# Optimization experiments

Measured on AMD Instinct MI355X. Metric: run time of the kernel, lower is better.

Reference implementation:

```python
import math
import jax, jax.numpy as jnp
import numpy as np

NUM_HEADS = 12
NUM_LANDMARKS = 32

def iterative_inv(mat, n_iter=6):
    # mat: [B, H, m, m] row-stochastic kernel; Newton-Schulz pseudo-inverse
    m = mat.shape[-1]
    I = jnp.eye(m, dtype=mat.dtype)
    K = mat
    # 'else' branch: per-(B,H) normalization by max column sum
    denom = jnp.max(jnp.sum(K, axis=-2), axis=-1)[..., None, None]
    V = jnp.swapaxes(K, -1, -2) / denom
    for _ in range(n_iter):
        KV = jnp.matmul(K, V)
        V = jnp.matmul(0.25 * V, 13.0 * I - jnp.matmul(KV, 15.0 * I - jnp.matmul(KV, 7.0 * I - KV)))
    return V

def setup_inputs() -> dict:
    key = jax.random.key(0)
    k1, k2, k3 = jax.random.split(key, 3)
    B, N, C = 8, 2048, 768
    x = jax.random.normal(k1, (B, N, C), dtype=jnp.float32)
    w_qkv = jax.random.normal(k2, (C, 3 * C), dtype=jnp.float32) * (1.0 / math.sqrt(C))
    w_proj = jax.random.normal(k3, (C, C), dtype=jnp.float32) * (1.0 / math.sqrt(C))
    b_proj = jnp.zeros((C,), dtype=jnp.float32)
    return {"x": x, "w_qkv": w_qkv, "w_proj": w_proj, "b_proj": b_proj}

def reference(x, w_qkv, w_proj, b_proj):
    B, N, C = x.shape
    H = NUM_HEADS
    d = C // H
    m = NUM_LANDMARKS
    qkv = (x @ w_qkv).reshape(B, N, 3, H, d).transpose(2, 0, 3, 1, 4)  # [3,B,H,N,d]
    Q, K, V = qkv[0], qkv[1], qkv[2]
    scale = 1.0 / math.sqrt(math.sqrt(d))
    Q = Q * scale
    K = K * scale
    # landmark pooling: mean over contiguous chunks of size N//m
    Q_l = Q.reshape(B, H, m, N // m, d).mean(axis=-2)  # [B,H,m,d]
    K_l = K.reshape(B, H, m, N // m, d).mean(axis=-2)
    kernel_1 = jax.nn.softmax(jnp.einsum('bhnd,bhmd->bhnm', Q, K_l), axis=-1)   # [B,H,N,m]
    kernel_2 = jax.nn.softmax(jnp.einsum('bhmd,bhkd->bhmk', Q_l, K_l), axis=-1) # [B,H,m,m]
    kernel_3 = jax.nn.softmax(jnp.einsum('bhmd,bhnd->bhmn', Q_l, K), axis=-1)   # [B,H,m,N]
    X = jnp.matmul(jnp.matmul(kernel_1, iterative_inv(kernel_2)), jnp.matmul(kernel_3, V))  # [B,H,N,d]
    X = X.transpose(0, 2, 1, 3).reshape(B, N, C)
    return X @ w_proj + b_proj
```

## Files before the change

### kernel.cpp

```cpp
#include <hip/hip_runtime.h>
#include <hip/hip_bf16.h>

typedef __hip_bfloat16 bf16;
typedef __attribute__((ext_vector_type(8))) __bf16 bf16x8;
typedef __attribute__((ext_vector_type(4))) float f32x4;

#define NB 8
#define SEQ 2048
#define CH 768
#define NH 12
#define HD 64
#define NL 32
#define BHT (NB*NH)
#define TOK (NB*SEQ)
#define QK_SCALE 0.35355339059327379f

#define BAR() __builtin_amdgcn_s_barrier()
#define WLGKM0() __asm__ __volatile__("s_waitcnt lgkmcnt(0)" ::: "memory")
#define WVM(n) __asm__ __volatile__("s_waitcnt vmcnt(" #n ")" ::: "memory")

__device__ __forceinline__ void async_ld16(const bf16* g, bf16* l) {
    unsigned loff = (unsigned)__builtin_amdgcn_readfirstlane((int)(unsigned)(uintptr_t)l);
    __builtin_amdgcn_global_load_lds(
        (const __attribute__((address_space(1))) unsigned*)(uintptr_t)g,
        (__attribute__((address_space(3))) unsigned*)(uintptr_t)loff, 16, 0, 0);
}

__global__ void convert_x(const float* __restrict__ x, bf16* __restrict__ xb) {
    size_t i = ((size_t)blockIdx.x * 256 + threadIdx.x) * 8;
    float4 a = *reinterpret_cast<const float4*>(x + i);
    float4 b = *reinterpret_cast<const float4*>(x + i + 4);
    alignas(16) bf16 tmp[8];
    tmp[0] = __float2bfloat16(a.x); tmp[1] = __float2bfloat16(a.y);
    tmp[2] = __float2bfloat16(a.z); tmp[3] = __float2bfloat16(a.w);
    tmp[4] = __float2bfloat16(b.x); tmp[5] = __float2bfloat16(b.y);
    tmp[6] = __float2bfloat16(b.z); tmp[7] = __float2bfloat16(b.w);
    *reinterpret_cast<uint4*>(xb + i) = *reinterpret_cast<const uint4*>(tmp);
}

__global__ void transpose_f32(const float* __restrict__ in, bf16* __restrict__ outp,
                              int Hrows, int Wcols) {
    __shared__ float tile[32][33];
    int bx = blockIdx.x * 32, by = blockIdx.y * 32;
    int tx = threadIdx.x, ty = threadIdx.y;
    for (int i = 0; i < 32; i += 8)
        tile[ty + i][tx] = in[(size_t)(by + ty + i) * Wcols + bx + tx];
    __syncthreads();
    for (int i = 0; i < 32; i += 8)
        outp[(size_t)(bx + ty + i) * Hrows + by + tx] = __float2bfloat16(tile[tx][ty + i]);
}

template <int EPI>
__global__ __launch_bounds__(512, 2) void gemm_bt(
    const bf16* __restrict__ A, const bf16* __restrict__ Bt,
    int Nout, int Kdim,
    bf16* __restrict__ q, bf16* __restrict__ k, bf16* __restrict__ vt,
    float* __restrict__ Ql, float* __restrict__ Kl,
    float* __restrict__ outp, const float* __restrict__ bias_f) {
    __shared__ __align__(16) bf16 As[2][256 * 64];
    __shared__ __align__(16) bf16 Bs[2][256 * 64];
    const int t = threadIdx.x;
    const int wave = t >> 6, lane = t & 63;
    const int quad = lane >> 4, l15 = lane & 15;
    const int wr = wave >> 2, wc = wave & 3;

    int p = blockIdx.y * gridDim.x + blockIdx.x;
    int xcd = p & 7, j = p >> 3;
    int gx = gridDim.x;
    int bn = j % gx;
    int bm = (j / gx) * 8 + xcd;
    const int bm0 = bm * 256;
    const int bn0 = bn * 256;

    const int T = Kdim >> 6;

    const int srow = t >> 3;
    const int scol = (((t & 7) ^ (srow & 7)) << 3);
    const bf16* Abase = A + (size_t)(bm0 + srow) * Kdim + scol;
    const bf16* Bbase = Bt + (size_t)(bn0 + srow) * Kdim + scol;

    auto stageA = [&](int kt, int hf) {
        const bf16* g = Abase + (size_t)(hf * 128) * Kdim + kt * 64;
        bf16* l = &As[kt & 1][hf * 8192 + t * 8];
        async_ld16(g, l);
        async_ld16(g + (size_t)64 * Kdim, l + 4096);
    };
    auto stageB = [&](int kt, int hf) {
        const bf16* g = Bbase + (size_t)(hf * 128) * Kdim + kt * 64;
        bf16* l = &Bs[kt & 1][hf * 8192 + t * 8];
        async_ld16(g, l);
        async_ld16(g + (size_t)64 * Kdim, l + 4096);
    };

    const int swk[2] = { (quad ^ (l15 & 7)) << 3, ((4 + quad) ^ (l15 & 7)) << 3 };
    const bf16* arow = &As[0][wr * 8192 + l15 * 64];
    const bf16* brow = &Bs[0][(wc >> 1) * 8192 + ((wc & 1) * 64 + l15) * 64];

    f32x4 acc[8][4];
    const f32x4 zero4 = {0.f, 0.f, 0.f, 0.f};
    #pragma unroll
    for (int i = 0; i < 8; i++)
        #pragma unroll
        for (int jj = 0; jj < 4; jj++) acc[i][jj] = zero4;

    stageA(0, 0); stageA(0, 1); stageB(0, 0); stageB(0, 1);
    if (T > 1) {
        stageB(1, 0); stageB(1, 1);
        WVM(4);
    } else {
        WVM(0);
    }
    BAR();

    bf16x8 a[4][2], b[4][2];
    #pragma unroll 2
    for (int kt = 0; kt < T; kt++) {
        const int cur = kt & 1;
        const bf16* ab = arow + cur * 16384;
        const bf16* bb = brow + cur * 16384;

        #pragma unroll
        for (int mi = 0; mi < 4; mi++)
            #pragma unroll
            for (int kk = 0; kk < 2; kk++)
                a[mi][kk] = *reinterpret_cast<const bf16x8*>(ab + mi * 1024 + swk[kk]);
        #pragma unroll
        for (int ni = 0; ni < 2; ni++)
            #pragma unroll
            for (int kk = 0; kk < 2; kk++)
                b[ni][kk] = *reinterpret_cast<const bf16x8*>(bb + ni * 1024 + swk[kk]);
        if (kt + 1 < T) stageA(kt + 1, 0);
        BAR(); WLGKM0();
        __builtin_amdgcn_s_setprio(1);
        #pragma unroll
        for (int mi = 0; mi < 4; mi++)
            #pragma unroll
            for (int ni = 0; ni < 2; ni++)
                #pragma unroll
                for (int kk = 0; kk < 2; kk++)
                    acc[mi][ni] = __builtin_amdgcn_mfma_f32_16x16x32_bf16(a[mi][kk], b[ni][kk], acc[mi][ni], 0, 0, 0);
        __builtin_amdgcn_s_setprio(0);
        BAR();

        #pragma unroll
        for (int ni = 2; ni < 4; ni++)
            #pragma unroll
            for (int kk = 0; kk < 2; kk++)
                b[ni][kk] = *reinterpret_cast<const bf16x8*>(bb + ni * 1024 + swk[kk]);
        if (kt + 1 < T) stageA(kt + 1, 1);
        BAR(); WLGKM0();
        __builtin_amdgcn_s_setprio(1);
        #pragma unroll
        for (int mi = 0; mi < 4; mi++)
            #pragma unroll
            for (int ni = 2; ni < 4; ni++)
                #pragma unroll
                for (int kk = 0; kk < 2; kk++)
                    acc[mi][ni] = __builtin_amdgcn_mfma_f32_16x16x32_bf16(a[mi][kk], b[ni][kk], acc[mi][ni], 0, 0, 0);
        __builtin_amdgcn_s_setprio(0);
        BAR();

        #pragma unroll
        for (int mi = 0; mi < 4; mi++)
            #pragma unroll
            for (int kk = 0; kk < 2; kk++)
                a[mi][kk] = *reinterpret_cast<const bf16x8*>(ab + (mi + 4) * 1024 + swk[kk]);
        if (kt + 2 < T) stageB(kt + 2, 0);
        BAR(); WLGKM0();
        __builtin_amdgcn_s_setprio(1);
        #pragma unroll
        for (int mi = 0; mi < 4; mi++)
            #pragma unroll
            for (int ni = 0; ni < 2; ni++)
                #pragma unroll
                for (int kk = 0; kk < 2; kk++)
                    acc[mi + 4][ni] = __builtin_amdgcn_mfma_f32_16x16x32_bf16(a[mi][kk], b[ni][kk], acc[mi + 4][ni], 0, 0, 0);
        __builtin_amdgcn_s_setprio(0);
        BAR();

        if (kt + 2 < T) stageB(kt + 2, 1);
        BAR(); WLGKM0();
        __builtin_amdgcn_s_setprio(1);
        #pragma unroll
        for (int mi = 0; mi < 4; mi++)
            #pragma unroll
            for (int ni = 2; ni < 4; ni++)
                #pragma unroll
                for (int kk = 0; kk < 2; kk++)
                    acc[mi + 4][ni] = __builtin_amdgcn_mfma_f32_16x16x32_bf16(a[mi][kk], b[ni][kk], acc[mi + 4][ni], 0, 0, 0);
        __builtin_amdgcn_s_setprio(0);
        if (kt + 2 < T) {
            WVM(4);
        } else if (kt + 1 < T) {
            WVM(0);
        }
        BAR();
    }

    if (EPI == 0) {
        const int which = bn0 / CH;
        const int rem0 = bn0 - which * CH + wc * 64;
        const int b = bm0 >> 11;
        const int h = rem0 >> 6;
        const int bh = b * NH + h;
        const int nnb = (bm0 & 2047) + wr * 128;
        if (which < 2) {
            bf16* dstqk = (which == 0) ? q : k;
            float* dstl = (which == 0) ? Ql : Kl;
            const int la0 = nnb >> 6;
            #pragma unroll
            for (int hf = 0; hf < 2; hf++) {
                #pragma unroll
                for (int ni = 0; ni < 4; ni++) {
                    int dd = ni * 16 + l15;
                    float colsum = 0.f;
                    #pragma unroll
                    for (int m2 = 0; m2 < 4; m2++) {
                        int mi = hf * 4 + m2;
                        int nn0 = nnb + mi * 16 + quad * 4;
                        #pragma unroll
                        for (int r = 0; r < 4; r++) {
                            float val = acc[mi][ni][r];
                            colsum += val;
                            dstqk[((size_t)bh * SEQ + nn0 + r) * HD + dd] = __float2bfloat16(val * QK_SCALE);
                        }
                    }
                    colsum += __shfl_xor(colsum, 16);
                    colsum += __shfl_xor(colsum, 32);
                    if (quad == 0)
                        dstl[((size_t)bh * NL + la0 + hf) * HD + dd] = colsum * (QK_SCALE / 64.f);
                }
            }
        } else {
            #pragma unroll
            for (int ni = 0; ni < 4; ni++) {
                int dd = ni * 16 + l15;
                #pragma unroll
                for (int mi = 0; mi < 8; mi++) {
                    int nn0 = nnb + mi * 16 + quad * 4;
                    alignas(8) bf16 four[4];
                    #pragma unroll
                    for (int r = 0; r < 4; r++) four[r] = __float2bfloat16(acc[mi][ni][r]);
                    *reinterpret_cast<uint2*>(&vt[((size_t)bh * HD + dd) * SEQ + nn0]) =
                        *reinterpret_cast<const uint2*>(four);
                }
            }
        }
    } else {
        #pragma unroll
        for (int ni = 0; ni < 4; ni++) {
            int col = bn0 + wc * 64 + ni * 16 + l15;
            float bb = bias_f[col];
            #pragma unroll
            for (int mi = 0; mi < 8; mi++)
                #pragma unroll
                for (int r = 0; r < 4; r++) {
                    int row = bm0 + wr * 128 + mi * 16 + quad * 4 + r;
                    outp[(size_t)row * Nout + col] = acc[mi][ni][r] + bb;
                }
        }
    }
}

__global__ __launch_bounds__(256) void k3_pv(const float* __restrict__ Ql,
                                             const bf16* __restrict__ Kb,
                                             const bf16* __restrict__ Vt,
                                             float* __restrict__ Opart,
                                             float* __restrict__ Spart) {
    __shared__ __align__(16) bf16 Pw[4][32 * 136];
    __shared__ __align__(16) float Ored[4][32 * 65];
    __shared__ float Sred[4 * 32];
    const int bh = blockIdx.x, cc = blockIdx.y;
    const int n0 = cc * 512;
    const int t = threadIdx.x;
    const int w = t >> 6, lane = t & 63;
    const int quad = lane >> 4, l15 = lane & 15;

    const bf16* Kbh = Kb + (size_t)bh * SEQ * HD;
    const bf16* Vtb = Vt + (size_t)bh * HD * SEQ;

    bf16x8 af[2][2];
    #pragma unroll
    for (int mt = 0; mt < 2; mt++)
        #pragma unroll
        for (int kh = 0; kh < 2; kh++) {
            const float* src = Ql + (size_t)bh * NL * HD + (mt * 16 + l15) * 64 + kh * 32 + quad * 8;
            alignas(16) bf16 tmp[8];
            #pragma unroll
            for (int jj = 0; jj < 8; jj++) tmp[jj] = __float2bfloat16(src[jj]);
            af[mt][kh] = *reinterpret_cast<const bf16x8*>(tmp);
        }

    const f32x4 zero4 = {0.f, 0.f, 0.f, 0.f};
    f32x4 oacc[2][4];
    #pragma unroll
    for (int mt = 0; mt < 2; mt++)
        #pragma unroll
        for (int nd = 0; nd < 4; nd++) oacc[mt][nd] = zero4;
    float rs[2][4];
    #pragma unroll
    for (int mt = 0; mt < 2; mt++)
        #pragma unroll
        for (int r = 0; r < 4; r++) rs[mt][r] = 0.f;

    bf16* Pme = &Pw[w][0];

    #pragma unroll
    for (int h = 0; h < 2; h++) {
        f32x4 sacc[2][4];
        #pragma unroll
        for (int mt = 0; mt < 2; mt++)
            #pragma unroll
            for (int nt = 0; nt < 4; nt++) sacc[mt][nt] = zero4;
        #pragma unroll
        for (int nt = 0; nt < 4; nt++) {
            int n = n0 + w * 128 + h * 64 + nt * 16 + l15;
            bf16x8 kf0 = *reinterpret_cast<const bf16x8*>(&Kbh[(size_t)n * HD + quad * 8]);
            bf16x8 kf1 = *reinterpret_cast<const bf16x8*>(&Kbh[(size_t)n * HD + 32 + quad * 8]);
            #pragma unroll
            for (int mt = 0; mt < 2; mt++) {
                sacc[mt][nt] = __builtin_amdgcn_mfma_f32_16x16x32_bf16(af[mt][0], kf0, sacc[mt][nt], 0, 0, 0);
                sacc[mt][nt] = __builtin_amdgcn_mfma_f32_16x16x32_bf16(af[mt][1], kf1, sacc[mt][nt], 0, 0, 0);
            }
        }
        #pragma unroll
        for (int mt = 0; mt < 2; mt++)
            #pragma unroll
            for (int nt = 0; nt < 4; nt++)
                #pragma unroll
                for (int r = 0; r < 4; r++) {
                    float pv = __expf(sacc[mt][nt][r]);
                    rs[mt][r] += pv;
                    int row = mt * 16 + quad * 4 + r;
                    Pme[row * 136 + h * 64 + nt * 16 + l15] = __float2bfloat16(pv);
                }
    }
    __asm__ __volatile__("s_waitcnt lgkmcnt(0)" ::: "memory");

    #pragma unroll
    for (int kt = 0; kt < 4; kt++) {
        bf16x8 pa[2];
        pa[0] = *reinterpret_cast<const bf16x8*>(&Pme[l15 * 136 + kt * 32 + quad * 8]);
        pa[1] = *reinterpret_cast<const bf16x8*>(&Pme[(16 + l15) * 136 + kt * 32 + quad * 8]);
        int kbase = n0 + w * 128 + kt * 32 + quad * 8;
        #pragma unroll
        for (int nd = 0; nd < 4; nd++) {
            bf16x8 bv = *reinterpret_cast<const bf16x8*>(&Vtb[(size_t)(nd * 16 + l15) * SEQ + kbase]);
            oacc[0][nd] = __builtin_amdgcn_mfma_f32_16x16x32_bf16(pa[0], bv, oacc[0][nd], 0, 0, 0);
            oacc[1][nd] = __builtin_amdgcn_mfma_f32_16x16x32_bf16(pa[1], bv, oacc[1][nd], 0, 0, 0);
        }
    }

    #pragma unroll
    for (int mt = 0; mt < 2; mt++)
        #pragma unroll
        for (int r = 0; r < 4; r++) {
            float v = rs[mt][r];
            #pragma unroll
            for (int o = 1; o < 16; o <<= 1) v += __shfl_xor(v, o);
            rs[mt][r] = v;
        }
    if (l15 == 0)
        #pragma unroll
        for (int mt = 0; mt < 2; mt++)
            #pragma unroll
            for (int r = 0; r < 4; r++)
                Sred[w * 32 + mt * 16 + quad * 4 + r] = rs[mt][r];
    #pragma unroll
    for (int mt = 0; mt < 2; mt++)
        #pragma unroll
        for (int nd = 0; nd < 4; nd++)
            #pragma unroll
            for (int r = 0; r < 4; r++)
                Ored[w][(mt * 16 + quad * 4 + r) * 65 + nd * 16 + l15] = oacc[mt][nd][r];
    __syncthreads();

    float* Op = Opart + ((size_t)bh * 4 + cc) * (NL * HD);
    for (int e = t; e < 2048; e += 256) {
        int m = e >> 6, dd = e & 63;
        Op[e] = Ored[0][m * 65 + dd] + Ored[1][m * 65 + dd] +
                Ored[2][m * 65 + dd] + Ored[3][m * 65 + dd];
    }
    if (t < 32)
        Spart[((size_t)bh * 4 + cc) * NL + t] = Sred[t] + Sred[32 + t] + Sred[64 + t] + Sred[96 + t];
}

__device__ inline void mm32(float* Cm, const float* Am, const float* Bm, int t) {
    for (int e = t; e < 1024; e += 256) {
        int i = e >> 5, jj = e & 31;
        float s = 0.f;
        #pragma unroll
        for (int kk = 0; kk < 32; kk++) s += Am[i * 32 + kk] * Bm[kk * 32 + jj];
        Cm[e] = s;
    }
}

__global__ __launch_bounds__(256) void newton_inv(const float* __restrict__ Ql,
                                                  const float* __restrict__ Kl,
                                                  const float* __restrict__ Opart,
                                                  const float* __restrict__ Spart,
                                                  float* __restrict__ W2) {
    __shared__ float K2[1024], Vv[1024], KV[1024], Ta[1024], Tb[1024];
    __shared__ float K3[2048];
    __shared__ float stot[32];
    __shared__ float red[32];
    __shared__ float denom_s;
    int bh = blockIdx.x;
    int t = threadIdx.x;
    const float* ql = Ql + (size_t)bh * NL * HD;
    const float* kl = Kl + (size_t)bh * NL * HD;

    if (t < 32) {
        const float* sp = Spart + (size_t)bh * 4 * NL;
        stot[t] = sp[t] + sp[32 + t] + sp[64 + t] + sp[96 + t];
    }
    {
        const float* op = Opart + (size_t)bh * 4 * (NL * HD);
        for (int e = t; e < 2048; e += 256)
            K3[e] = op[e] + op[2048 + e] + op[4096 + e] + op[6144 + e];
    }

    for (int e = t; e < 1024; e += 256) {
        int i = e >> 5, jj = e & 31;
        float s = 0.f;
        #pragma unroll 8
        for (int d = 0; d < 64; d++) s += ql[i * 64 + d] * kl[jj * 64 + d];
        K2[e] = s;
    }
    __syncthreads();
    for (int e = t; e < 2048; e += 256) K3[e] *= (1.f / stot[e >> 6]);
    if (t < 32) {
        float mx = -1e30f;
        for (int jj = 0; jj < 32; jj++) mx = fmaxf(mx, K2[t * 32 + jj]);
        float sm = 0.f;
        for (int jj = 0; jj < 32; jj++) { float e = __expf(K2[t * 32 + jj] - mx); K2[t * 32 + jj] = e; sm += e; }
        float inv = 1.f / sm;
        for (int jj = 0; jj < 32; jj++) K2[t * 32 + jj] *= inv;
    }
    __syncthreads();
    if (t < 32) {
        float cs = 0.f;
        for (int i = 0; i < 32; i++) cs += K2[i * 32 + t];
        red[t] = cs;
    }
    __syncthreads();
    if (t == 0) {
        float mx = red[0];
        for (int jj = 1; jj < 32; jj++) mx = fmaxf(mx, red[jj]);
        denom_s = mx;
    }
    __syncthreads();
    float invden = 1.f / denom_s;
    for (int e = t; e < 1024; e += 256) {
        int i = e >> 5, jj = e & 31;
        Vv[e] = K2[jj * 32 + i] * invden;
    }
    __syncthreads();
    for (int it = 0; it < 6; it++) {
        mm32(KV, K2, Vv, t);
        __syncthreads();
        for (int e = t; e < 1024; e += 256) { int i = e >> 5, jj = e & 31; Ta[e] = ((i == jj) ? 7.f : 0.f) - KV[e]; }
        __syncthreads();
        mm32(Tb, KV, Ta, t);
        __syncthreads();
        for (int e = t; e < 1024; e += 256) { int i = e >> 5, jj = e & 31; Tb[e] = ((i == jj) ? 15.f : 0.f) - Tb[e]; }
        __syncthreads();
        mm32(Ta, KV, Tb, t);
        __syncthreads();
        for (int e = t; e < 1024; e += 256) { int i = e >> 5, jj = e & 31; Ta[e] = ((i == jj) ? 13.f : 0.f) - Ta[e]; }
        __syncthreads();
        mm32(Tb, Vv, Ta, t);
        __syncthreads();
        for (int e = t; e < 1024; e += 256) Vv[e] = 0.25f * Tb[e];
        __syncthreads();
    }
    for (int e = t; e < 2048; e += 256) {
        int i = e >> 6, dd = e & 63;
        float s = 0.f;
        #pragma unroll
        for (int kk = 0; kk < 32; kk++) s += Vv[i * 32 + kk] * K3[kk * 64 + dd];
        W2[(size_t)bh * NL * HD + e] = s;
    }
}

__global__ __launch_bounds__(256) void rows_fused(const bf16* __restrict__ Qb,
                                                  const float* __restrict__ Kl,
                                                  const float* __restrict__ W2,
                                                  bf16* __restrict__ Xp) {
    __shared__ __align__(16) bf16 Klb[32 * 64];
    __shared__ __align__(16) bf16 W2t[64 * 32];
    __shared__ __align__(16) bf16 Pw[4][32 * 40];
    const int bh = blockIdx.x, tile = blockIdx.y;
    const int t = threadIdx.x, w = t >> 6, lane = t & 63;
    const int quad = lane >> 4, l15 = lane & 15;

    {
        const float* ksrc = Kl + (size_t)bh * NL * HD;
        const float* wsrc = W2 + (size_t)bh * NL * HD;
        int e0 = t * 8;
        #pragma unroll
        for (int jj = 0; jj < 8; jj++) {
            int e = e0 + jj;
            Klb[e] = __float2bfloat16(ksrc[e]);
            int kk = e >> 6, dd = e & 63;
            W2t[dd * 32 + kk] = __float2bfloat16(wsrc[e]);
        }
    }
    __syncthreads();

    const int b = bh / NH, h = bh - b * NH;
    const int row0 = tile * 128 + w * 32;
    const bf16* qbase = Qb + ((size_t)bh * SEQ + row0) * HD;

    const f32x4 zero4 = {0.f, 0.f, 0.f, 0.f};
    f32x4 sacc[2][2];
    #pragma unroll
    for (int mt = 0; mt < 2; mt++)
        #pragma unroll
        for (int nt = 0; nt < 2; nt++) sacc[mt][nt] = zero4;
    #pragma unroll
    for (int kh = 0; kh < 2; kh++) {
        bf16x8 bk0 = *reinterpret_cast<const bf16x8*>(&Klb[(l15) * 64 + kh * 32 + quad * 8]);
        bf16x8 bk1 = *reinterpret_cast<const bf16x8*>(&Klb[(16 + l15) * 64 + kh * 32 + quad * 8]);
        #pragma unroll
        for (int mt = 0; mt < 2; mt++) {
            bf16x8 aq = *reinterpret_cast<const bf16x8*>(&qbase[(size_t)(mt * 16 + l15) * HD + kh * 32 + quad * 8]);
            sacc[mt][0] = __builtin_amdgcn_mfma_f32_16x16x32_bf16(aq, bk0, sacc[mt][0], 0, 0, 0);
            sacc[mt][1] = __builtin_amdgcn_mfma_f32_16x16x32_bf16(aq, bk1, sacc[mt][1], 0, 0, 0);
        }
    }

    float invs[2][4];
    bf16* Pme = &Pw[w][0];
    #pragma unroll
    for (int mt = 0; mt < 2; mt++)
        #pragma unroll
        for (int r = 0; r < 4; r++) {
            float v0 = __expf(sacc[mt][0][r]);
            float v1 = __expf(sacc[mt][1][r]);
            int row = mt * 16 + quad * 4 + r;
            Pme[row * 40 + l15] = __float2bfloat16(v0);
            Pme[row * 40 + 16 + l15] = __float2bfloat16(v1);
            float v = v0 + v1;
            #pragma unroll
            for (int o = 1; o < 16; o <<= 1) v += __shfl_xor(v, o);
            invs[mt][r] = 1.f / v;
        }
    __asm__ __volatile__("s_waitcnt lgkmcnt(0)" ::: "memory");

    f32x4 oacc[2][4];
    #pragma unroll
    for (int mt = 0; mt < 2; mt++)
        #pragma unroll
        for (int nd = 0; nd < 4; nd++) oacc[mt][nd] = zero4;
    bf16x8 pa[2];
    pa[0] = *reinterpret_cast<const bf16x8*>(&Pme[l15 * 40 + quad * 8]);
    pa[1] = *reinterpret_cast<const bf16x8*>(&Pme[(16 + l15) * 40 + quad * 8]);
    #pragma unroll
    for (int nd = 0; nd < 4; nd++) {
        bf16x8 bw = *reinterpret_cast<const bf16x8*>(&W2t[(nd * 16 + l15) * 32 + quad * 8]);
        oacc[0][nd] = __builtin_amdgcn_mfma_f32_16x16x32_bf16(pa[0], bw, oacc[0][nd], 0, 0, 0);
        oacc[1][nd] = __builtin_amdgcn_mfma_f32_16x16x32_bf16(pa[1], bw, oacc[1][nd], 0, 0, 0);
    }

    #pragma unroll
    for (int mt = 0; mt < 2; mt++)
        #pragma unroll
        for (int nd = 0; nd < 4; nd++)
            #pragma unroll
            for (int r = 0; r < 4; r++) {
                int row = row0 + mt * 16 + quad * 4 + r;
                Xp[((size_t)(b * SEQ + row)) * CH + h * 64 + nd * 16 + l15] =
                    __float2bfloat16(oacc[mt][nd][r] * invs[mt][r]);
            }
}

extern "C" void kernel_launch(void* const* d_in, const int* in_sizes, int n_in,
                              void* d_out, int out_size, void* d_ws, size_t ws_size,
                              hipStream_t stream) {
    const float* x      = (const float*)d_in[0];
    const float* w_qkv  = (const float*)d_in[1];
    const float* w_proj = (const float*)d_in[2];
    const float* b_proj = (const float*)d_in[3];
    float* out = (float*)d_out;

    char* ws = (char*)d_ws;
    size_t off = 0;
    auto alloc = [&](size_t bytes) -> void* {
        void* p = ws + off;
        off += (bytes + 255) & ~(size_t)255;
        return p;
    };
    bf16* wqkvT  = (bf16*)alloc((size_t)3 * CH * CH * 2);
    bf16* wprojT = (bf16*)alloc((size_t)CH * CH * 2);
    bf16* Qb     = (bf16*)alloc((size_t)BHT * SEQ * HD * 2);
    bf16* Kb     = (bf16*)alloc((size_t)BHT * SEQ * HD * 2);
    bf16* Vt     = (bf16*)alloc((size_t)BHT * SEQ * HD * 2);
    float* Ql    = (float*)alloc((size_t)BHT * NL * HD * 4);
    float* Kl    = (float*)alloc((size_t)BHT * NL * HD * 4);
    float* Opart = (float*)alloc((size_t)BHT * 4 * NL * HD * 4);
    float* Spart = (float*)alloc((size_t)BHT * 4 * NL * 4);
    float* W2    = (float*)alloc((size_t)BHT * NL * HD * 4);
    bf16* Xp     = (bf16*)alloc((size_t)TOK * CH * 2);
    if (ws_size < off) return;
    bf16* xb = Xp;

    convert_x<<<TOK * CH / 2048, 256, 0, stream>>>(x, xb);
    transpose_f32<<<dim3((3 * CH) / 32, CH / 32), dim3(32, 8), 0, stream>>>(w_qkv, wqkvT, CH, 3 * CH);
    transpose_f32<<<dim3(CH / 32, CH / 32), dim3(32, 8), 0, stream>>>(w_proj, wprojT, CH, CH);

    gemm_bt<0><<<dim3((3 * CH) / 256, TOK / 256), 512, 0, stream>>>(
        xb, wqkvT, 3 * CH, CH, Qb, Kb, Vt, Ql, Kl, nullptr, nullptr);

    k3_pv<<<dim3(BHT, 4), 256, 0, stream>>>(Ql, Kb, Vt, Opart, Spart);
    newton_inv<<<BHT, 256, 0, stream>>>(Ql, Kl, Opart, Spart, W2);
    rows_fused<<<dim3(BHT, SEQ / 128), 256, 0, stream>>>(Qb, Kl, W2, Xp);

    gemm_bt<1><<<dim3(CH / 256, TOK / 256), 512, 0, stream>>>(
        Xp, wprojT, CH, CH, nullptr, nullptr, nullptr, nullptr, nullptr, out, b_proj);
}
```

Before: 284.3 us.

## Use 256x192 GEMM tiles and move Newton inverse into the k3_pv launch

The GEMM N-tile drops from 256 to 192 columns, with a single-stage prefetch pipeline and per-fragment head index computation in the epilogue. This changes the grid shape, giving more blocks for wave balancing on the QKV and projection GEMMs. The Newton-Schulz inverse now runs as an extra blockIdx.y slice of k3_pv, so it executes alongside the PV partial sums instead of serially in newton_inv. A small combine kernel then only does the reduction and the W2 product. In exchange the GEMM gets less reuse per B tile and a restructured wait/barrier schedule, and the launch needs an extra workspace buffer.

```diff
diff --git a/kernel.cpp b/kernel.cpp
--- a/kernel.cpp
+++ b/kernel.cpp
@@ -58,7 +58,7 @@
     float* __restrict__ Ql, float* __restrict__ Kl,
     float* __restrict__ outp, const float* __restrict__ bias_f) {
     __shared__ __align__(16) bf16 As[2][256 * 64];
-    __shared__ __align__(16) bf16 Bs[2][256 * 64];
+    __shared__ __align__(16) bf16 Bs[2][192 * 64];
     const int t = threadIdx.x;
     const int wave = t >> 6, lane = t & 63;
     const int quad = lane >> 4, l15 = lane & 15;
@@ -70,7 +70,7 @@
     int bn = j % gx;
     int bm = (j / gx) * 8 + xcd;
     const int bm0 = bm * 256;
-    const int bn0 = bn * 256;
+    const int bn0 = bn * 192;
 
     const int T = Kdim >> 6;
 
@@ -79,45 +79,37 @@
     const bf16* Abase = A + (size_t)(bm0 + srow) * Kdim + scol;
     const bf16* Bbase = Bt + (size_t)(bn0 + srow) * Kdim + scol;
 
-    auto stageA = [&](int kt, int hf) {
-        const bf16* g = Abase + (size_t)(hf * 128) * Kdim + kt * 64;
-        bf16* l = &As[kt & 1][hf * 8192 + t * 8];
-        async_ld16(g, l);
-        async_ld16(g + (size_t)64 * Kdim, l + 4096);
+    auto stA = [&](int kt, int c) {
+        async_ld16(Abase + (size_t)(c * 64) * Kdim + kt * 64,
+                   &As[kt & 1][c * 4096 + t * 8]);
     };
-    auto stageB = [&](int kt, int hf) {
-        const bf16* g = Bbase + (size_t)(hf * 128) * Kdim + kt * 64;
-        bf16* l = &Bs[kt & 1][hf * 8192 + t * 8];
-        async_ld16(g, l);
-        async_ld16(g + (size_t)64 * Kdim, l + 4096);
+    auto stB = [&](int kt, int c) {
+        async_ld16(Bbase + (size_t)(c * 64) * Kdim + kt * 64,
+                   &Bs[kt & 1][c * 4096 + t * 8]);
     };
 
     const int swk[2] = { (quad ^ (l15 & 7)) << 3, ((4 + quad) ^ (l15 & 7)) << 3 };
-    const bf16* arow = &As[0][wr * 8192 + l15 * 64];
-    const bf16* brow = &Bs[0][(wc >> 1) * 8192 + ((wc & 1) * 64 + l15) * 64];
-
-    f32x4 acc[8][4];
+    const bf16* arow = &As[0][(wr * 128 + l15) * 64];
+    const bf16* brow = &Bs[0][(wc * 48 + l15) * 64];
+
+    f32x4 acc[8][3];
     const f32x4 zero4 = {0.f, 0.f, 0.f, 0.f};
     #pragma unroll
     for (int i = 0; i < 8; i++)
         #pragma unroll
-        for (int jj = 0; jj < 4; jj++) acc[i][jj] = zero4;
-
-    stageA(0, 0); stageA(0, 1); stageB(0, 0); stageB(0, 1);
-    if (T > 1) {
-        stageB(1, 0); stageB(1, 1);
-        WVM(4);
-    } else {
-        WVM(0);
-    }
+        for (int jj = 0; jj < 3; jj++) acc[i][jj] = zero4;
+
+    stA(0, 0); stA(0, 2); stB(0, 0); stB(0, 1); stB(0, 2); stA(0, 1); stA(0, 3);
+    WVM(2);
     BAR();
 
-    bf16x8 a[4][2], b[4][2];
+    bf16x8 a[4][2], b[3][2];
     #pragma unroll 2
     for (int kt = 0; kt < T; kt++) {
         const int cur = kt & 1;
+        const bool nxt = (kt + 1 < T);
         const bf16* ab = arow + cur * 16384;
-        const bf16* bb = brow + cur * 16384;
+        const bf16* bb = brow + cur * 12288;
 
         #pragma unroll
         for (int mi = 0; mi < 4; mi++)
@@ -129,7 +121,7 @@
             #pragma unroll
             for (int kk = 0; kk < 2; kk++)
                 b[ni][kk] = *reinterpret_cast<const bf16x8*>(bb + ni * 1024 + swk[kk]);
-        if (kt + 1 < T) stageA(kt + 1, 0);
+        if (nxt) { stA(kt + 1, 0); stA(kt + 1, 2); }
         BAR(); WLGKM0();
         __builtin_amdgcn_s_setprio(1);
         #pragma unroll
@@ -143,21 +135,18 @@
         BAR();
 
         #pragma unroll
-        for (int ni = 2; ni < 4; ni++)
-            #pragma unroll
-            for (int kk = 0; kk < 2; kk++)
-                b[ni][kk] = *reinterpret_cast<const bf16x8*>(bb + ni * 1024 + swk[kk]);
-        if (kt + 1 < T) stageA(kt + 1, 1);
+        for (int kk = 0; kk < 2; kk++)
+            b[2][kk] = *reinterpret_cast<const bf16x8*>(bb + 2 * 1024 + swk[kk]);
+        if (nxt) { stB(kt + 1, 0); stB(kt + 1, 1); }
         BAR(); WLGKM0();
         __builtin_amdgcn_s_setprio(1);
         #pragma unroll
         for (int mi = 0; mi < 4; mi++)
             #pragma unroll
-            for (int ni = 2; ni < 4; ni++)
-                #pragma unroll
-                for (int kk = 0; kk < 2; kk++)
-                    acc[mi][ni] = __builtin_amdgcn_mfma_f32_16x16x32_bf16(a[mi][kk], b[ni][kk], acc[mi][ni], 0, 0, 0);
+            for (int kk = 0; kk < 2; kk++)
+                acc[mi][2] = __builtin_amdgcn_mfma_f32_16x16x32_bf16(a[mi][kk], b[2][kk], acc[mi][2], 0, 0, 0);
         __builtin_amdgcn_s_setprio(0);
+        if (nxt) { WVM(4); } else { WVM(0); }
         BAR();
 
         #pragma unroll
@@ -165,7 +154,7 @@
             #pragma unroll
             for (int kk = 0; kk < 2; kk++)
                 a[mi][kk] = *reinterpret_cast<const bf16x8*>(ab + (mi + 4) * 1024 + swk[kk]);
-        if (kt + 2 < T) stageB(kt + 2, 0);
+        if (nxt) { stB(kt + 1, 2); stA(kt + 1, 1); }
         BAR(); WLGKM0();
         __builtin_amdgcn_s_setprio(1);
         #pragma unroll
@@ -178,31 +167,23 @@
         __builtin_amdgcn_s_setprio(0);
         BAR();
 
-        if (kt + 2 < T) stageB(kt + 2, 1);
-        BAR(); WLGKM0();
+        if (nxt) { stA(kt + 1, 3); }
+        BAR();
         __builtin_amdgcn_s_setprio(1);
         #pragma unroll
         for (int mi = 0; mi < 4; mi++)
             #pragma unroll
-            for (int ni = 2; ni < 4; ni++)
-                #pragma unroll
-                for (int kk = 0; kk < 2; kk++)
-                    acc[mi + 4][ni] = __builtin_amdgcn_mfma_f32_16x16x32_bf16(a[mi][kk], b[ni][kk], acc[mi + 4][ni], 0, 0, 0);
+            for (int kk = 0; kk < 2; kk++)
+                acc[mi + 4][2] = __builtin_amdgcn_mfma_f32_16x16x32_bf16(a[mi][kk], b[2][kk], acc[mi + 4][2], 0, 0, 0);
         __builtin_amdgcn_s_setprio(0);
-        if (kt + 2 < T) {
-            WVM(4);
-        } else if (kt + 1 < T) {
-            WVM(0);
-        }
+        WVM(2);
         BAR();
     }
 
     if (EPI == 0) {
         const int which = bn0 / CH;
-        const int rem0 = bn0 - which * CH + wc * 64;
+        const int rem0 = bn0 - which * CH + wc * 48;
         const int b = bm0 >> 11;
-        const int h = rem0 >> 6;
-        const int bh = b * NH + h;
         const int nnb = (bm0 & 2047) + wr * 128;
         if (which < 2) {
             bf16* dstqk = (which == 0) ? q : k;
@@ -211,8 +192,11 @@
             #pragma unroll
             for (int hf = 0; hf < 2; hf++) {
                 #pragma unroll
-                for (int ni = 0; ni < 4; ni++) {
-                    int dd = ni * 16 + l15;
+                for (int ni = 0; ni < 3; ni++) {
+                    int rem = rem0 + ni * 16;
+                    int h = rem >> 6;
+                    int dd = (rem & 63) + l15;
+                    int bh = b * NH + h;
                     float colsum = 0.f;
                     #pragma unroll
                     for (int m2 = 0; m2 < 4; m2++) {
@@ -233,8 +217,11 @@
             }
         } else {
             #pragma unroll
-            for (int ni = 0; ni < 4; ni++) {
-                int dd = ni * 16 + l15;
+            for (int ni = 0; ni < 3; ni++) {
+                int rem = rem0 + ni * 16;
+                int h = rem >> 6;
+                int dd = (rem & 63) + l15;
+                int bh = b * NH + h;
                 #pragma unroll
                 for (int mi = 0; mi < 8; mi++) {
                     int nn0 = nnb + mi * 16 + quad * 4;
@@ -248,8 +235,8 @@
         }
     } else {
         #pragma unroll
-        for (int ni = 0; ni < 4; ni++) {
-            int col = bn0 + wc * 64 + ni * 16 + l15;
+        for (int ni = 0; ni < 3; ni++) {
+            int col = bn0 + wc * 48 + ni * 16 + l15;
             float bb = bias_f[col];
             #pragma unroll
             for (int mi = 0; mi < 8; mi++)
@@ -262,17 +249,100 @@
     }
 }
 
+__device__ inline void mm32(float* Cm, const float* Am, const float* Bm, int t) {
+    for (int e = t; e < 1024; e += 256) {
+        int i = e >> 5, jj = e & 31;
+        float s = 0.f;
+        #pragma unroll
+        for (int kk = 0; kk < 32; kk++) s += Am[i * 32 + kk] * Bm[kk * 32 + jj];
+        Cm[e] = s;
+    }
+}
+
 __global__ __launch_bounds__(256) void k3_pv(const float* __restrict__ Ql,
+                                             const float* __restrict__ Klm,
                                              const bf16* __restrict__ Kb,
                                              const bf16* __restrict__ Vt,
                                              float* __restrict__ Opart,
-                                             float* __restrict__ Spart) {
-    __shared__ __align__(16) bf16 Pw[4][32 * 136];
-    __shared__ __align__(16) float Ored[4][32 * 65];
-    __shared__ float Sred[4 * 32];
-    const int bh = blockIdx.x, cc = blockIdx.y;
+                                             float* __restrict__ Spart,
+                                             float* __restrict__ Vinv) {
+    __shared__ __align__(16) char smem[69632];
+    const int bh = blockIdx.x;
+    const int t = threadIdx.x;
+
+    if (blockIdx.y == 0) {
+        float* K2 = (float*)smem;
+        float* Vv = K2 + 1024;
+        float* KV = K2 + 2048;
+        float* Ta = K2 + 3072;
+        float* Tb = K2 + 4096;
+        float* red = K2 + 5120;
+        const float* ql = Ql + (size_t)bh * NL * HD;
+        const float* kl = Klm + (size_t)bh * NL * HD;
+
+        for (int e = t; e < 1024; e += 256) {
+            int i = e >> 5, jj = e & 31;
+            float s = 0.f;
+            #pragma unroll 8
+            for (int d = 0; d < 64; d++) s += ql[i * 64 + d] * kl[jj * 64 + d];
+            K2[e] = s;
+        }
+        __syncthreads();
+        if (t < 32) {
+            float mx = -1e30f;
+            for (int jj = 0; jj < 32; jj++) mx = fmaxf(mx, K2[t * 32 + jj]);
+            float sm = 0.f;
+            for (int jj = 0; jj < 32; jj++) { float e = __expf(K2[t * 32 + jj] - mx); K2[t * 32 + jj] = e; sm += e; }
+            float inv = 1.f / sm;
+            for (int jj = 0; jj < 32; jj++) K2[t * 32 + jj] *= inv;
+        }
+        __syncthreads();
+        if (t < 32) {
+            float cs = 0.f;
+            for (int i = 0; i < 32; i++) cs += K2[i * 32 + t];
+            red[t] = cs;
+        }
+        __syncthreads();
+        if (t == 0) {
+            float mx = red[0];
+            for (int jj = 1; jj < 32; jj++) mx = fmaxf(mx, red[jj]);
+            red[32] = mx;
+        }
+        __syncthreads();
+        float invden = 1.f / red[32];
+        for (int e = t; e < 1024; e += 256) {
+            int i = e >> 5, jj = e & 31;
+            Vv[e] = K2[jj * 32 + i] * invden;
+        }
+        __syncthreads();
+        for (int it = 0; it < 6; it++) {
+            mm32(KV, K2, Vv, t);
+            __syncthreads();
+            for (int e = t; e < 1024; e += 256) { int i = e >> 5, jj = e & 31; Ta[e] = ((i == jj) ? 7.f : 0.f) - KV[e]; }
+            __syncthreads();
+            mm32(Tb, KV, Ta, t);
+            __syncthreads();
+            for (int e = t; e < 1024; e += 256) { int i = e >> 5, jj = e & 31; Tb[e] = ((i == jj) ? 15.f : 0.f) - Tb[e]; }
+            __syncthreads();
+            mm32(Ta, KV, Tb, t);
+            __syncthreads();
+            for (int e = t; e < 1024; e += 256) { int i = e >> 5, jj = e & 31; Ta[e] = ((i == jj) ? 13.f : 0.f) - Ta[e]; }
+            __syncthreads();
+            mm32(Tb, Vv, Ta, t);
+            __syncthreads();
+            for (int e = t; e < 1024; e += 256) Vv[e] = 0.25f * Tb[e];
+            __syncthreads();
+        }
+        for (int e = t; e < 1024; e += 256)
+            Vinv[(size_t)bh * 1024 + e] = Vv[e];
+        return;
+    }
+
+    bf16* Pw0 = (bf16*)smem;
+    float* Ored0 = (float*)(smem + 34816);
+    float* Sred = (float*)(smem + 34816 + 33280);
+    const int cc = blockIdx.y - 1;
     const int n0 = cc * 512;
-    const int t = threadIdx.x;
     const int w = t >> 6, lane = t & 63;
     const int quad = lane >> 4, l15 = lane & 15;
 
@@ -303,7 +373,7 @@
         #pragma unroll
         for (int r = 0; r < 4; r++) rs[mt][r] = 0.f;
 
-    bf16* Pme = &Pw[w][0];
+    bf16* Pme = Pw0 + w * (32 * 136);
 
     #pragma unroll
     for (int h = 0; h < 2; h++) {
@@ -372,43 +442,28 @@
         for (int nd = 0; nd < 4; nd++)
             #pragma unroll
             for (int r = 0; r < 4; r++)
-                Ored[w][(mt * 16 + quad * 4 + r) * 65 + nd * 16 + l15] = oacc[mt][nd][r];
+                Ored0[w * (32 * 65) + (mt * 16 + quad * 4 + r) * 65 + nd * 16 + l15] = oacc[mt][nd][r];
     __syncthreads();
 
     float* Op = Opart + ((size_t)bh * 4 + cc) * (NL * HD);
     for (int e = t; e < 2048; e += 256) {
         int m = e >> 6, dd = e & 63;
-        Op[e] = Ored[0][m * 65 + dd] + Ored[1][m * 65 + dd] +
-                Ored[2][m * 65 + dd] + Ored[3][m * 65 + dd];
+        Op[e] = Ored0[0 * (32 * 65) + m * 65 + dd] + Ored0[1 * (32 * 65) + m * 65 + dd] +
+                Ored0[2 * (32 * 65) + m * 65 + dd] + Ored0[3 * (32 * 65) + m * 65 + dd];
     }
     if (t < 32)
         Spart[((size_t)bh * 4 + cc) * NL + t] = Sred[t] + Sred[32 + t] + Sred[64 + t] + Sred[96 + t];
 }
 
-__device__ inline void mm32(float* Cm, const float* Am, const float* Bm, int t) {
-    for (int e = t; e < 1024; e += 256) {
-        int i = e >> 5, jj = e & 31;
-        float s = 0.f;
-        #pragma unroll
-        for (int kk = 0; kk < 32; kk++) s += Am[i * 32 + kk] * Bm[kk * 32 + jj];
-        Cm[e] = s;
-    }
-}
-
-__global__ __launch_bounds__(256) void newton_inv(const float* __restrict__ Ql,
-                                                  const float* __restrict__ Kl,
-                                                  const float* __restrict__ Opart,
+__global__ __launch_bounds__(256) void combine_w2(const float* __restrict__ Opart,
                                                   const float* __restrict__ Spart,
+                                                  const float* __restrict__ Vinv,
                                                   float* __restrict__ W2) {
-    __shared__ float K2[1024], Vv[1024], KV[1024], Ta[1024], Tb[1024];
     __shared__ float K3[2048];
+    __shared__ float Vv[1024];
     __shared__ float stot[32];
-    __shared__ float red[32];
-    __shared__ float denom_s;
-    int bh = blockIdx.x;
-    int t = threadIdx.x;
-    const float* ql = Ql + (size_t)bh * NL * HD;
-    const float* kl = Kl + (size_t)bh * NL * HD;
+    const int bh = blockIdx.x;
+    const int t = threadIdx.x;
 
     if (t < 32) {
         const float* sp = Spart + (size_t)bh * 4 * NL;
@@ -419,61 +474,11 @@
         for (int e = t; e < 2048; e += 256)
             K3[e] = op[e] + op[2048 + e] + op[4096 + e] + op[6144 + e];
     }
-
-    for (int e = t; e < 1024; e += 256) {
-        int i = e >> 5, jj = e & 31;
-        float s = 0.f;
-        #pragma unroll 8
-        for (int d = 0; d < 64; d++) s += ql[i * 64 + d] * kl[jj * 64 + d];
-        K2[e] = s;
-    }
+    for (int e = t; e < 1024; e += 256)
+        Vv[e] = Vinv[(size_t)bh * 1024 + e];
     __syncthreads();
     for (int e = t; e < 2048; e += 256) K3[e] *= (1.f / stot[e >> 6]);
-    if (t < 32) {
-        float mx = -1e30f;
-        for (int jj = 0; jj < 32; jj++) mx = fmaxf(mx, K2[t * 32 + jj]);
-        float sm = 0.f;
-        for (int jj = 0; jj < 32; jj++) { float e = __expf(K2[t * 32 + jj] - mx); K2[t * 32 + jj] = e; sm += e; }
-        float inv = 1.f / sm;
-        for (int jj = 0; jj < 32; jj++) K2[t * 32 + jj] *= inv;
-    }
     __syncthreads();
-    if (t < 32) {
-        float cs = 0.f;
-        for (int i = 0; i < 32; i++) cs += K2[i * 32 + t];
-        red[t] = cs;
-    }
-    __syncthreads();
-    if (t == 0) {
-        float mx = red[0];
-        for (int jj = 1; jj < 32; jj++) mx = fmaxf(mx, red[jj]);
-        denom_s = mx;
-    }
-    __syncthreads();
-    float invden = 1.f / denom_s;
-    for (int e = t; e < 1024; e += 256) {
-        int i = e >> 5, jj = e & 31;
-        Vv[e] = K2[jj * 32 + i] * invden;
-    }
-    __syncthreads();
-    for (int it = 0; it < 6; it++) {
-        mm32(KV, K2, Vv, t);
-        __syncthreads();
-        for (int e = t; e < 1024; e += 256) { int i = e >> 5, jj = e & 31; Ta[e] = ((i == jj) ? 7.f : 0.f) - KV[e]; }
-        __syncthreads();
-        mm32(Tb, KV, Ta, t);
-        __syncthreads();
-        for (int e = t; e < 1024; e += 256) { int i = e >> 5, jj = e & 31; Tb[e] = ((i == jj) ? 15.f : 0.f) - Tb[e]; }
-        __syncthreads();
-        mm32(Ta, KV, Tb, t);
-        __syncthreads();
-        for (int e = t; e < 1024; e += 256) { int i = e >> 5, jj = e & 31; Ta[e] = ((i == jj) ? 13.f : 0.f) - Ta[e]; }
-        __syncthreads();
-        mm32(Tb, Vv, Ta, t);
-        __syncthreads();
-        for (int e = t; e < 1024; e += 256) Vv[e] = 0.25f * Tb[e];
-        __syncthreads();
-    }
     for (int e = t; e < 2048; e += 256) {
         int i = e >> 6, dd = e & 63;
         float s = 0.f;
@@ -600,6 +605,7 @@
     float* Kl    = (float*)alloc((size_t)BHT * NL * HD * 4);
     float* Opart = (float*)alloc((size_t)BHT * 4 * NL * HD * 4);
     float* Spart = (float*)alloc((size_t)BHT * 4 * NL * 4);
+    float* Vinv  = (float*)alloc((size_t)BHT * NL * NL * 4);
     float* W2    = (float*)alloc((size_t)BHT * NL * HD * 4);
     bf16* Xp     = (bf16*)alloc((size_t)TOK * CH * 2);
     if (ws_size < off) return;
@@ -609,13 +615,13 @@
     transpose_f32<<<dim3((3 * CH) / 32, CH / 32), dim3(32, 8), 0, stream>>>(w_qkv, wqkvT, CH, 3 * CH);
     transpose_f32<<<dim3(CH / 32, CH / 32), dim3(32, 8), 0, stream>>>(w_proj, wprojT, CH, CH);
 
-    gemm_bt<0><<<dim3((3 * CH) / 256, TOK / 256), 512, 0, stream>>>(
+    gemm_bt<0><<<dim3((3 * CH) / 192, TOK / 256), 512, 0, stream>>>(
         xb, wqkvT, 3 * CH, CH, Qb, Kb, Vt, Ql, Kl, nullptr, nullptr);
 
-    k3_pv<<<dim3(BHT, 4), 256, 0, stream>>>(Ql, Kb, Vt, Opart, Spart);
-    newton_inv<<<BHT, 256, 0, stream>>>(Ql, Kl, Opart, Spart, W2);
+    k3_pv<<<dim3(BHT, 5), 256, 0, stream>>>(Ql, Kl, Kb, Vt, Opart, Spart, Vinv);
+    combine_w2<<<BHT, 256, 0, stream>>>(Opart, Spart, Vinv, W2);
     rows_fused<<<dim3(BHT, SEQ / 128), 256, 0, stream>>>(Qb, Kl, W2, Xp);
 
-    gemm_bt<1><<<dim3(CH / 256, TOK / 256), 512, 0, stream>>>(
+    gemm_bt<1><<<dim3(CH / 192, TOK / 256), 512, 0, stream>>>(
         Xp, wprojT, CH, CH, nullptr, nullptr, nullptr, nullptr, nullptr, out, b_proj);
 }
```

Result: faster. 277.2 us (-2.5%).
